# Performance work log

Hardware: AMD Instinct MI355X
Metric: run time of the kernel (lower is better)

The kernel has to match this reference:

```python
import jax, jax.numpy as jnp
import numpy as np

DN = ('NCHW', 'OIHW', 'NCHW')
LAP = jnp.array([[0., -1., 0.], [-1., 4., -1.], [0., -1., 0.]], dtype=jnp.float32).reshape(1, 1, 3, 3)
CH, NE = 24, 256


def conv(x, w, stride=1, pad=0):
    return jax.lax.conv_general_dilated(x, w, (stride, stride), ((pad, pad), (pad, pad)), dimension_numbers=DN)


def conv_t(x, w):
    # torch ConvTranspose2d(k=4, s=2, p=1); w is torch layout [in, out, 4, 4]
    wt = jnp.flip(w, (2, 3)).transpose(1, 0, 2, 3)
    return jax.lax.conv_general_dilated(x, wt, (1, 1), ((2, 2), (2, 2)), lhs_dilation=(2, 2), dimension_numbers=DN)


def spatial_attn(x, w_sa):
    y = jnp.concatenate([jnp.mean(x, 1, keepdims=True), jnp.max(x, 1, keepdims=True)], 1)
    return x * jax.nn.sigmoid(conv(y, w_sa, pad=3))


def res_branch(x, wr, wp, wsa):
    k = wr.shape[-1]
    h = conv(x, wr, pad=k // 2)
    h = conv(h, wp)
    return jax.nn.relu(spatial_attn(h, wsa))


def enc_block(x, wr, wp, wsa, wout):
    x = x + res_branch(x, wr, wp, wsa)
    return conv(x, wout, stride=2, pad=1)


def dec_block(x, wr, wp, wsa, wout):
    x = conv_t(x, wout)
    return x + res_branch(x, wr, wp, wsa)


def quantize(inp, embed):
    # inp: [B,H,W,D] tokens, embed: [D,N] codebook
    f = inp.reshape(-1, inp.shape[-1])
    dist = (f * f).sum(1, keepdims=True) - 2.0 * (f @ embed) + (embed * embed).sum(0, keepdims=True)
    ind = jnp.argmin(dist, axis=1)
    q = jnp.take(embed.T, ind, axis=0).reshape(inp.shape)
    diff = jnp.mean((jax.lax.stop_gradient(q) - inp) ** 2)
    q = inp + jax.lax.stop_gradient(q - inp)  # straight-through
    return q, diff


def _forward(x, w_img_in, w_img_out,
             w_res_et, w_pw_et, w_sa_et, w_out_et,
             w_res_em, w_pw_em, w_sa_em, w_out_em,
             w_res_ed, w_pw_ed, w_sa_ed, w_out_ed,
             w_res_dt, w_pw_dt, w_sa_dt, w_out_dt,
             w_res_dm, w_pw_dm, w_sa_dm, w_out_dm,
             w_res_dd, w_pw_dd, w_sa_dd, w_out_dd,
             w_squ1, w_squ2, embed2, embed3):
    xl = jax.lax.stop_gradient(conv(jnp.mean(x, 1, keepdims=True), LAP, pad=1))
    h = conv(xl, w_img_in)
    enc1 = enc_block(h, w_res_et, w_pw_et, w_sa_et, w_out_et)      # H/2
    enc2 = enc_block(enc1, w_res_em, w_pw_em, w_sa_em, w_out_em)   # H/4
    enc3 = enc_block(enc2, w_res_ed, w_pw_ed, w_sa_ed, w_out_ed)   # H/8
    qt2, d2 = quantize(enc2.transpose(0, 2, 3, 1), embed2)
    qt2 = qt2.transpose(0, 3, 1, 2)
    qt3, d3 = quantize(enc3.transpose(0, 2, 3, 1), embed3)
    qt3 = qt3.transpose(0, 3, 1, 2)
    dec3 = dec_block(qt3, w_res_dd, w_pw_dd, w_sa_dd, w_out_dd)    # H/4
    dec2 = conv(jnp.concatenate([dec3, qt2], 1), w_squ2)
    dec2 = dec_block(dec2, w_res_dm, w_pw_dm, w_sa_dm, w_out_dm)   # H/2
    dec1 = conv(jnp.concatenate([dec2, enc1], 1), w_squ1)
    dec1 = dec_block(dec1, w_res_dt, w_pw_dt, w_sa_dt, w_out_dt)   # H
    mask_lap = conv(dec1, w_img_out)
    clean_lap = xl - mask_lap
    return mask_lap, clean_lap, (d2 + d3).reshape(1)


def _param_shapes():
    shapes = {'w_img_in': (CH, 1, 1, 1), 'w_img_out': (1, CH, 1, 1),
              'w_squ1': (CH, 2 * CH, 1, 1), 'w_squ2': (CH, 2 * CH, 1, 1),
              'embed2': (CH, NE), 'embed3': (CH, NE)}
    for tag, k in [('et', 7), ('em', 5), ('ed', 3), ('dt', 7), ('dm', 5), ('dd', 3)]:
        shapes['w_res_' + tag] = (CH, CH, k, k)
        shapes['w_pw_' + tag] = (CH, CH, 1, 1)
        shapes['w_sa_' + tag] = (1, 2, 7, 7)
        shapes['w_out_' + tag] = (CH, CH, 4, 4)
    return shapes


def setup_inputs() -> dict:
    key = jax.random.key(0)
    shapes = _param_shapes()
    names = sorted(shapes)
    keys = jax.random.split(key, len(names) + 1)
    inputs = {'x': jax.random.normal(keys[0], (8, 3, 512, 512), dtype=jnp.float32)}
    for k_, name in zip(keys[1:], names):
        w = jax.random.normal(k_, shapes[name], dtype=jnp.float32)
        if not name.startswith('embed'):
            w = w * 0.05  # conv weight init scale
        inputs[name] = w
    return inputs


def reference(x, embed2, embed3, w_img_in, w_img_out,
              w_out_dd, w_out_dm, w_out_dt, w_out_ed, w_out_em, w_out_et,
              w_pw_dd, w_pw_dm, w_pw_dt, w_pw_ed, w_pw_em, w_pw_et,
              w_res_dd, w_res_dm, w_res_dt, w_res_ed, w_res_em, w_res_et,
              w_sa_dd, w_sa_dm, w_sa_dt, w_sa_ed, w_sa_em, w_sa_et,
              w_squ1, w_squ2):
    return _forward(x, w_img_in, w_img_out,
                    w_res_et, w_pw_et, w_sa_et, w_out_et,
                    w_res_em, w_pw_em, w_sa_em, w_out_em,
                    w_res_ed, w_pw_ed, w_sa_ed, w_out_ed,
                    w_res_dt, w_pw_dt, w_sa_dt, w_out_dt,
                    w_res_dm, w_pw_dm, w_sa_dm, w_out_dm,
                    w_res_dd, w_pw_dd, w_sa_dd, w_out_dd,
                    w_squ1, w_squ2, embed2, embed3)
```

## Files before the change

kernel.cpp:

```cpp
#include <hip/hip_runtime.h>
#include <math.h>

#define CH 24

typedef __attribute__((ext_vector_type(8))) short short8v;
typedef __attribute__((ext_vector_type(4))) float f32x4;
typedef unsigned short ushort_t;
typedef unsigned int uint_t;

__device__ inline ushort_t bf16r(float f){
  uint_t u = __float_as_uint(f);
  u += 0x7FFF + ((u>>16)&1);
  return (ushort_t)(u>>16);
}
__device__ inline float bf2f(uint_t u){ return __uint_as_float(u<<16); }

__global__ void k_r_res(const float* __restrict__ w, float* __restrict__ wT, int K){
  int i = blockIdx.x*256 + threadIdx.x;
  int n = 576*K*K; if (i >= n) return;
  int co = i % 24, ci = (i/24) % 24, kk = i/576;
  int ky = kk / K, kx = kk % K;
  wT[i] = w[((co*24+ci)*K+ky)*K+kx];
}
__global__ void k_r_pw(const float* __restrict__ w, float* __restrict__ wT, int CIN){
// ... 123 lines not shown
    for (int reg=0; reg<4; reg++){
      float v0 = acc[i][0][reg], v1 = acc[i][1][reg];
      float v0n = __shfl_xor(v0, 1, 64);
      float v1n = __shfl_xor(v1, 1, 64);
      int pxr = kg*4 + reg;
      uint_t packed; int uidx;
      if ((li & 1) == 0){
        packed = (uint_t)bf16r(v0) | ((uint_t)bf16r(v0n) << 16);
        uidx = li >> 1;
      } else {
        packed = (uint_t)bf16r(v1n) | ((uint_t)bf16r(v1) << 16);
        uidx = 8 + (li >> 1);
      }
      s[pxr*20 + uidx] = packed;
    }
    __asm__ volatile("s_waitcnt lgkmcnt(0)" ::: "memory");
    __builtin_amdgcn_sched_barrier(0);
    short8v a2 = *(const short8v*)((const ushort_t*)s + li*40 + kg*8);
    f32x4 d0 = __builtin_amdgcn_mfma_f32_16x16x32_bf16(a2, bpw0, zero, 0, 0, 0);
    f32x4 d1 = __builtin_amdgcn_mfma_f32_16x16x32_bf16(a2, bpw1, zero, 0, 0, 0);
    int gy = blockIdx.y*16 + wid + (i&1)*8;
    int gx = blockIdx.x*32 + (i>>1)*16 + kg*4;
    if (OUTBF){
      uint2 p0; p0.x = (uint_t)bf16r(d0[0]) | ((uint_t)bf16r(d0[1])<<16);
      p0.y = (uint_t)bf16r(d0[2]) | ((uint_t)bf16r(d0[3])<<16);
      *(uint2*)(outb_b + (size_t)li*HW + (size_t)gy*W + gx) = p0;
      if (li < 8){
        uint2 p1; p1.x = (uint_t)bf16r(d1[0]) | ((uint_t)bf16r(d1[1])<<16);
        p1.y = (uint_t)bf16r(d1[2]) | ((uint_t)bf16r(d1[3])<<16);
        *(uint2*)(outb_b + (size_t)(16+li)*HW + (size_t)gy*W + gx) = p1;
      }
    } else {
      *(f32x4*)(outb_f + (size_t)li*HW + (size_t)gy*W + gx) = d0;
      if (li < 8)
        *(f32x4*)(outb_f + (size_t)(16+li)*HW + (size_t)gy*W + gx) = d1;
    }
    f32x4 sm, mx;
    #pragma unroll
    for (int reg=0; reg<4; reg++){
      sm[reg] = d0[reg] + d1[reg];
      mx[reg] = fmaxf(d0[reg], (li<8) ? d1[reg] : -3.4e38f);
    }
    #pragma unroll
    for (int m=1; m<16; m<<=1){
      #pragma unroll
      for (int reg=0; reg<4; reg++){
        sm[reg] += __shfl_xor(sm[reg], m, 64);
        mx[reg] = fmaxf(mx[reg], __shfl_xor(mx[reg], m, 64));
      }
    }
    if (li == 0){
      f32x4 me; me[0]=sm[0]*(1.f/24.f); me[1]=sm[1]*(1.f/24.f); me[2]=sm[2]*(1.f/24.f); me[3]=sm[3]*(1.f/24.f);
      *(f32x4*)(mmb + (size_t)gy*W + gx) = me;
      *(f32x4*)(mmb + (size_t)HW + (size_t)gy*W + gx) = mx;
    }
  }
}

template<bool INBF, bool OUTBF>
__launch_bounds__(512)
__global__ void k_convT_mfma(const void* in, const ushort_t* __restrict__ wb,
                             void* out, int Ho, int Wo, int istrIn, int istrOut){
  const int Hi = Ho>>1, Wi = Wo>>1;
  constexpr int SW_T = 18, NPX = 180;
  __shared__ ushort_t lds[NPX*24];
  int tid = threadIdx.x;
  const float* inb_f = (const float*)in + (size_t)blockIdx.z*istrIn;
  const ushort_t* inb_b = (const ushort_t*)in + (size_t)blockIdx.z*istrIn;
  int X0 = blockIdx.x*32, Y0 = blockIdx.y*16;
  int ix0 = (X0>>1) - 1, iy0 = (Y0>>1) - 1;
  int HWi = Hi*Wi;
  for (int i = tid; i < NPX*3; i += 512){
    int q = i / NPX;
    int pp = i - q*NPX;
    int row = pp / SW_T, col = pp - row*SW_T;
    int gy = iy0 + row, gx = ix0 + col;
    uint4 w4; w4.x=0u; w4.y=0u; w4.z=0u; w4.w=0u;
    if (gy>=0 && gy<Hi && gx>=0 && gx<Wi){
      size_t base = (size_t)gy*Wi + gx;
      int c0 = q*8;
      if (INBF){
        uint_t u0=inb_b[(size_t)(c0+0)*HWi+base], u1=inb_b[(size_t)(c0+1)*HWi+base];
        uint_t u2=inb_b[(size_t)(c0+2)*HWi+base], u3=inb_b[(size_t)(c0+3)*HWi+base];
        uint_t u4=inb_b[(size_t)(c0+4)*HWi+base], u5=inb_b[(size_t)(c0+5)*HWi+base];
        uint_t u6=inb_b[(size_t)(c0+6)*HWi+base], u7=inb_b[(size_t)(c0+7)*HWi+base];
        w4.x = u0 | (u1<<16); w4.y = u2 | (u3<<16); w4.z = u4 | (u5<<16); w4.w = u6 | (u7<<16);
      } else {
        w4.x = (uint_t)bf16r(inb_f[(size_t)(c0+0)*HWi+base]) | ((uint_t)bf16r(inb_f[(size_t)(c0+1)*HWi+base])<<16);
        w4.y = (uint_t)bf16r(inb_f[(size_t)(c0+2)*HWi+base]) | ((uint_t)bf16r(inb_f[(size_t)(c0+3)*HWi+base])<<16);
        w4.z = (uint_t)bf16r(inb_f[(size_t)(c0+4)*HWi+base]) | ((uint_t)bf16r(inb_f[(size_t)(c0+5)*HWi+base])<<16);
        w4.w = (uint_t)bf16r(inb_f[(size_t)(c0+6)*HWi+base]) | ((uint_t)bf16r(inb_f[(size_t)(c0+7)*HWi+base])<<16);
      }
    }
    *(uint4*)(lds + (size_t)pp*24 + q*8) = w4;
  }
  __syncthreads();
  int l = tid & 63, wid = tid >> 6;
  int kg = l >> 4, li = l & 15;
  int kgc = (kg < 3) ? kg : 2;
  f32x4 zero = {0.f,0.f,0.f,0.f};
  f32x4 acc[4][2];
  #pragma unroll
  for (int i=0;i<4;i++){ acc[i][0]=zero; acc[i][1]=zero; }

  const ushort_t* aln = lds + li*24 + kgc*8;

  #pragma unroll
  for (int i=0;i<4;i++){
    int g = wid + 8*i;
    int r = g & 15, q = g >> 4;
    int ky0 = (r+1)&1;
    #pragma unroll
    for (int t2=0;t2<2;t2++){
      int ky = ky0 + 2*t2;
      int liy = ((r+1-ky)>>1) + 1;
      #pragma unroll
      for (int u=0;u<2;u++){
        int kx = (q ? 0 : 1) + 2*u;
        int lixb = ((q+1-kx)>>1) + 1;
        int tap = ky*4 + kx;
        const ushort_t* wp = wb + (size_t)tap*1024;
        short8v b0 = *(const short8v*)(wp + l*8);
        short8v b1 = *(const short8v*)(wp + 512 + l*8);
        short8v a = *(const short8v*)(aln + (liy*SW_T + lixb)*24);
        acc[i][0] = __builtin_amdgcn_mfma_f32_16x16x32_bf16(a, b0, acc[i][0], 0, 0, 0);
        acc[i][1] = __builtin_amdgcn_mfma_f32_16x16x32_bf16(a, b1, acc[i][1], 0, 0, 0);
      }
    }
  }
  float* outb_f = (float*)out + (size_t)blockIdx.z*istrOut;
  ushort_t* outb_b = (ushort_t*)out + (size_t)blockIdx.z*istrOut;
  int HWo = Ho*Wo;
  #pragma unroll
  for (int i=0;i<4;i++){
    int g = wid + 8*i;
    int r = g & 15, q = g >> 4;
    int oy = Y0 + r;
    #pragma unroll
    for (int reg=0; reg<4; reg++){
      int ox = X0 + 2*(kg*4 + reg) + q;
      if (OUTBF){
        outb_b[(size_t)li*HWo + (size_t)oy*Wo + ox] = bf16r(acc[i][0][reg]);
        if (li < 8)
          outb_b[(size_t)(16+li)*HWo + (size_t)oy*Wo + ox] = bf16r(acc[i][1][reg]);
      } else {
        outb_f[(size_t)li*HWo + (size_t)oy*Wo + ox] = acc[i][0][reg];
        if (li < 8)
          outb_f[(size_t)(16+li)*HWo + (size_t)oy*Wo + ox] = acc[i][1][reg];
      }
    }
  }
}

template<bool INBF>
__launch_bounds__(512)
__global__ void k_down_mfma(const void* in, const ushort_t* __restrict__ wb,
                            float* __restrict__ out, int Ho, int Wo, int istrIn, int istrOut){
  const int Hi = Ho*2, Wi = Wo*2;
  constexpr int NPX = 18*34;
  __shared__ ushort_t lds[NPX*24];
  int tid = threadIdx.x;
  const float* inb_f = (const float*)in + (size_t)blockIdx.z*istrIn;
  const ushort_t* inb_b = (const ushort_t*)in + (size_t)blockIdx.z*istrIn;
  int X0 = blockIdx.x*16, Y0 = blockIdx.y*8;
  int ix0 = 2*X0 - 1, iy0 = 2*Y0 - 1;
  int HWi = Hi*Wi;
  for (int i = tid; i < NPX*3; i += 512){
    int q = i / NPX;
    int pp = i - q*NPX;
    int row = pp / 34;
    int rem = pp - row*34;
    int par = (rem >= 17) ? 1 : 0;
    int sub = rem - par*17;
    int gx = ix0 + 2*sub + par;
    int gy = iy0 + row;
    uint4 w4; w4.x=0u; w4.y=0u; w4.z=0u; w4.w=0u;
    if (gy>=0 && gy<Hi && gx>=0 && gx<Wi){
      size_t base = (size_t)gy*Wi + gx;
      int c0 = q*8;
      if (INBF){
        uint_t u0=inb_b[(size_t)(c0+0)*HWi+base], u1=inb_b[(size_t)(c0+1)*HWi+base];
        uint_t u2=inb_b[(size_t)(c0+2)*HWi+base], u3=inb_b[(size_t)(c0+3)*HWi+base];
        uint_t u4=inb_b[(size_t)(c0+4)*HWi+base], u5=inb_b[(size_t)(c0+5)*HWi+base];
        uint_t u6=inb_b[(size_t)(c0+6)*HWi+base], u7=inb_b[(size_t)(c0+7)*HWi+base];
        w4.x = u0 | (u1<<16); w4.y = u2 | (u3<<16); w4.z = u4 | (u5<<16); w4.w = u6 | (u7<<16);
      } else {
        w4.x = (uint_t)bf16r(inb_f[(size_t)(c0+0)*HWi+base]) | ((uint_t)bf16r(inb_f[(size_t)(c0+1)*HWi+base])<<16);
        w4.y = (uint_t)bf16r(inb_f[(size_t)(c0+2)*HWi+base]) | ((uint_t)bf16r(inb_f[(size_t)(c0+3)*HWi+base])<<16);
        w4.z = (uint_t)bf16r(inb_f[(size_t)(c0+4)*HWi+base]) | ((uint_t)bf16r(inb_f[(size_t)(c0+5)*HWi+base])<<16);
        w4.w = (uint_t)bf16r(inb_f[(size_t)(c0+6)*HWi+base]) | ((uint_t)bf16r(inb_f[(size_t)(c0+7)*HWi+base])<<16);
      }
    }
    *(uint4*)(lds + (size_t)pp*24 + q*8) = w4;
  }
  __syncthreads();
  int l = tid & 63, wid = tid >> 6;
  int kg = l >> 4, li = l & 15;
  int kgc = (kg < 3) ? kg : 2;
  f32x4 zero = {0.f,0.f,0.f,0.f};
  f32x4 acc0 = zero, acc1 = zero;
  const ushort_t* aln = lds + li*24 + kgc*8 + (size_t)(2*wid)*34*24;
  #pragma unroll
  for (int ky=0; ky<4; ky++){
    #pragma unroll
    for (int kx=0; kx<4; kx++){
      int tap = ky*4 + kx;
      const ushort_t* wp = wb + (size_t)tap*1024;
      short8v b0 = *(const short8v*)(wp + l*8);
      short8v b1 = *(const short8v*)(wp + 512 + l*8);
      short8v a = *(const short8v*)(aln + (ky*34 + (kx&1)*17 + (kx>>1))*24);
      acc0 = __builtin_amdgcn_mfma_f32_16x16x32_bf16(a, b0, acc0, 0, 0, 0);
      acc1 = __builtin_amdgcn_mfma_f32_16x16x32_bf16(a, b1, acc1, 0, 0, 0);
    }
  }
  int HWo = Ho*Wo;
  float* outb = out + (size_t)blockIdx.z*istrOut;
  int oy = Y0 + wid, ox = X0 + kg*4;
  float* o0 = outb + (size_t)li*HWo + (size_t)oy*Wo + ox;
  *(f32x4*)o0 = acc0;
  if (li < 8){
    float* o1 = outb + (size_t)(16+li)*HWo + (size_t)oy*Wo + ox;
    *(f32x4*)o1 = acc1;
  }
}

template<int K, int TH>
__launch_bounds__(256)
__global__ void k_conv(const float* __restrict__ in, const float* __restrict__ wT,
                       float* __restrict__ out, int H, int W, int istrIn, int istrOut){
  constexpr int TW = 32;
  constexpr int PX = (TW*TH)/256;
  constexpr int XT = TW/PX;
  constexpr int SW = TW + K - 1;
  constexpr int SWP = SW | 1;
  constexpr int SH = TH + K - 1;
  constexpr int CC = 8;
  __shared__ float tile[CC*SH*SWP];
  int tx = threadIdx.x % XT, ty = threadIdx.x / XT;
  int x0 = blockIdx.x*TW - K/2, y0 = blockIdx.y*TH - K/2;
  const float* inb = in + (size_t)blockIdx.z*istrIn;
  float acc[CH][PX];
  #pragma unroll
  for (int co=0;co<CH;co++)
    #pragma unroll
    for (int px=0;px<PX;px++) acc[co][px] = 0.f;

  #pragma unroll 1
  for (int c0=0;c0<CH;c0+=CC){
    __syncthreads();
    for (int i=threadIdx.x; i<CC*SH*SW; i+=256){
      int col = i % SW; int rr = i / SW; int row = rr % SH; int c = rr / SH;
      int gy = y0+row, gx = x0+col;
      tile[(c*SH+row)*SWP+col] = (gy>=0 && gy<H && gx>=0 && gx<W)
          ? inb[(size_t)(c0+c)*H*W + (size_t)gy*W + gx] : 0.f;
    }
    __syncthreads();
    #pragma unroll 1
    for (int ci=0;ci<CC;ci++){
      #pragma unroll 1
      for (int ky=0;ky<K;ky++){
        const float* trow = &tile[(ci*SH + ty+ky)*SWP + tx*PX];
        #pragma unroll
        for (int kx=0;kx<K;kx++){
          float v[PX];
          #pragma unroll
          for (int px=0;px<PX;px++) v[px] = trow[kx+px];
          const float* wp = wT + ((ky*K+kx)*24 + c0+ci)*24;
          #pragma unroll
          for (int co=0;co<CH;co++){
            float wv = wp[co];
            #pragma unroll
            for (int px=0;px<PX;px++) acc[co][px] = fmaf(v[px], wv, acc[co][px]);
          }
        }
      }
    }
  }
  int oy = blockIdx.y*TH+ty, ox = blockIdx.x*TW+tx*PX;
  float* ob = out + (size_t)blockIdx.z*istrOut + (size_t)oy*W + ox;
  #pragma unroll
  for (int co=0;co<CH;co++){
    if (PX == 2){
      float2 o; o.x=acc[co][0]; o.y=acc[co][1];
      *(float2*)(ob + (size_t)co*H*W) = o;
    } else {
      ob[(size_t)co*H*W] = acc[co][0];
    }
  }
}

__global__ void k_pw(const float* in, const float* __restrict__ wT,
                     float* out, float* __restrict__ mm, int HW, int istr, int istrMM){
  int p = (blockIdx.x*256 + threadIdx.x)*4;
  if (p >= HW) return;
  const float* ib = in + (size_t)blockIdx.z*istr;
  float acc[CH][4];
  #pragma unroll
  for (int co=0;co<CH;co++){ acc[co][0]=0;acc[co][1]=0;acc[co][2]=0;acc[co][3]=0; }
  #pragma unroll 1
  for (int ci=0;ci<CH;ci++){
    float4 v = *(const float4*)(ib + (size_t)ci*HW + p);
    const float* wp = wT + ci*24;
    #pragma unroll
    for (int co=0;co<CH;co++){
      float wv = wp[co];
      acc[co][0] = fmaf(v.x, wv, acc[co][0]);
      acc[co][1] = fmaf(v.y, wv, acc[co][1]);
      acc[co][2] = fmaf(v.z, wv, acc[co][2]);
      acc[co][3] = fmaf(v.w, wv, acc[co][3]);
    }
  }
  float mean[4]={0,0,0,0}, mx[4]={-3.4e38f,-3.4e38f,-3.4e38f,-3.4e38f};
  #pragma unroll
  for (int co=0;co<CH;co++)
    #pragma unroll
    for (int j=0;j<4;j++){ mean[j]+=acc[co][j]; mx[j]=fmaxf(mx[j],acc[co][j]); }
  float* ob = out + (size_t)blockIdx.z*istr;
  #pragma unroll
  for (int co=0;co<CH;co++){
    float4 o; o.x=acc[co][0]; o.y=acc[co][1]; o.z=acc[co][2]; o.w=acc[co][3];
    *(float4*)(ob + (size_t)co*HW + p) = o;
  }
  float* mb = mm + (size_t)blockIdx.z*istrMM;
  float4 me; me.x=mean[0]*(1.f/24.f); me.y=mean[1]*(1.f/24.f); me.z=mean[2]*(1.f/24.f); me.w=mean[3]*(1.f/24.f);
  float4 mxo; mxo.x=mx[0]; mxo.y=mx[1]; mxo.z=mx[2]; mxo.w=mx[3];
  *(float4*)(mb + p) = me;
  *(float4*)(mb + HW + p) = mxo;
}

template<bool BF>
__global__ void k_attn_res(const void* R_, const float* __restrict__ M,
                           const void* X_, const float* __restrict__ wsa,
                           void* out_, int H, int W, int istr, int istrMM){
  int p = (blockIdx.x*256 + threadIdx.x)*4;
  int HW = H*W;
  if (p >= HW) return;
  int py = p / W, px0 = p % W;
  const float* Mb = M + (size_t)blockIdx.z*istrMM;
  float s[4]={0,0,0,0};
  #pragma unroll
  for (int cc=0;cc<2;cc++){
    const float* Mc = Mb + (size_t)cc*HW;
    #pragma unroll 1
    for (int ky=0;ky<7;ky++){
      int gy = py+ky-3;
      if (gy<0||gy>=H) continue;
      const float* mr = Mc + (size_t)gy*W;
      float mv[10];
      #pragma unroll
      for (int j=0;j<10;j++){
        int gx = px0-3+j;
        mv[j] = (gx>=0 && gx<W) ? mr[gx] : 0.f;
      }
      const float* wr = wsa + (cc*7+ky)*7;
      #pragma unroll
      for (int kx=0;kx<7;kx++){
        float wv = wr[kx];
        #pragma unroll
        for (int px=0;px<4;px++) s[px] = fmaf(mv[kx+px], wv, s[px]);
      }
    }
  }
  float g[4];
  #pragma unroll
  for (int px=0;px<4;px++) g[px] = 1.f/(1.f+expf(-s[px]));
  #pragma unroll
  for (int c=0;c<CH;c++){
    float r0,r1,r2,r3, x0v,x1v,x2v,x3v;
    if (BF){
      const ushort_t* Rb = (const ushort_t*)R_ + (size_t)blockIdx.z*istr + (size_t)c*HW + p;
      const ushort_t* Xb = (const ushort_t*)X_ + (size_t)blockIdx.z*istr + (size_t)c*HW + p;
      uint2 rv = *(const uint2*)Rb;
      uint2 xv = *(const uint2*)Xb;
      r0=bf2f(rv.x&0xffffu); r1=bf2f(rv.x>>16); r2=bf2f(rv.y&0xffffu); r3=bf2f(rv.y>>16);
      x0v=bf2f(xv.x&0xffffu); x1v=bf2f(xv.x>>16); x2v=bf2f(xv.y&0xffffu); x3v=bf2f(xv.y>>16);
    } else {
      const float* Rb = (const float*)R_ + (size_t)blockIdx.z*istr + (size_t)c*HW + p;
      const float* Xb = (const float*)X_ + (size_t)blockIdx.z*istr + (size_t)c*HW + p;
      float4 rv = *(const float4*)Rb;
      float4 xv = *(const float4*)Xb;
      r0=rv.x; r1=rv.y; r2=rv.z; r3=rv.w;
      x0v=xv.x; x1v=xv.y; x2v=xv.z; x3v=xv.w;
    }
    float o0 = x0v + fmaxf(r0*g[0], 0.f);
    float o1 = x1v + fmaxf(r1*g[1], 0.f);
    float o2 = x2v + fmaxf(r2*g[2], 0.f);
    float o3 = x3v + fmaxf(r3*g[3], 0.f);
    if (BF){
      ushort_t* Ob = (ushort_t*)out_ + (size_t)blockIdx.z*istr + (size_t)c*HW + p;
      uint2 ov;
      ov.x = (uint_t)bf16r(o0) | ((uint_t)bf16r(o1)<<16);
      ov.y = (uint_t)bf16r(o2) | ((uint_t)bf16r(o3)<<16);
      *(uint2*)Ob = ov;
    } else {
      float* Ob = (float*)out_ + (size_t)blockIdx.z*istr + (size_t)c*HW + p;
      float4 ov; ov.x=o0; ov.y=o1; ov.z=o2; ov.w=o3;
      *(float4*)Ob = ov;
    }
  }
}

template<bool BF>
__global__ void k_attn_res_x(const void* R_, const float* __restrict__ M,
                             const float* __restrict__ XL, const float* __restrict__ wsa,
                             const float* __restrict__ wexp,
                             void* out_, int H, int W, int istr, int istrMM){
  int p = (blockIdx.x*256 + threadIdx.x)*4;
  int HW = H*W;
  if (p >= HW) return;
  int py = p / W, px0 = p % W;
  const float* Mb = M + (size_t)blockIdx.z*istrMM;
  float s[4]={0,0,0,0};
  #pragma unroll
  for (int cc=0;cc<2;cc++){
    const float* Mc = Mb + (size_t)cc*HW;
    #pragma unroll 1
    for (int ky=0;ky<7;ky++){
      int gy = py+ky-3;
      if (gy<0||gy>=H) continue;
      const float* mr = Mc + (size_t)gy*W;
      float mv[10];
      #pragma unroll
      for (int j=0;j<10;j++){
        int gx = px0-3+j;
        mv[j] = (gx>=0 && gx<W) ? mr[gx] : 0.f;
      }
      const float* wr = wsa + (cc*7+ky)*7;
      #pragma unroll
      for (int kx=0;kx<7;kx++){
        float wv = wr[kx];
        #pragma unroll
        for (int px=0;px<4;px++) s[px] = fmaf(mv[kx+px], wv, s[px]);
      }
    }
  }
  float g[4];
  #pragma unroll
  for (int px=0;px<4;px++) g[px] = 1.f/(1.f+expf(-s[px]));
  float4 xl4 = *(const float4*)(XL + (size_t)blockIdx.z*HW + p);
  #pragma unroll
  for (int c=0;c<CH;c++){
    float wc = wexp[c];
    float r0,r1,r2,r3;
    if (BF){
      const ushort_t* Rb = (const ushort_t*)R_ + (size_t)blockIdx.z*istr + (size_t)c*HW + p;
      uint2 rv = *(const uint2*)Rb;
      r0=bf2f(rv.x&0xffffu); r1=bf2f(rv.x>>16); r2=bf2f(rv.y&0xffffu); r3=bf2f(rv.y>>16);
    } else {
      const float* Rb = (const float*)R_ + (size_t)blockIdx.z*istr + (size_t)c*HW + p;
      float4 rv = *(const float4*)Rb;
      r0=rv.x; r1=rv.y; r2=rv.z; r3=rv.w;
    }
    float o0 = xl4.x*wc + fmaxf(r0*g[0], 0.f);
    float o1 = xl4.y*wc + fmaxf(r1*g[1], 0.f);
    float o2 = xl4.z*wc + fmaxf(r2*g[2], 0.f);
    float o3 = xl4.w*wc + fmaxf(r3*g[3], 0.f);
    if (BF){
      ushort_t* Ob = (ushort_t*)out_ + (size_t)blockIdx.z*istr + (size_t)c*HW + p;
      uint2 ov;
      ov.x = (uint_t)bf16r(o0) | ((uint_t)bf16r(o1)<<16);
      ov.y = (uint_t)bf16r(o2) | ((uint_t)bf16r(o3)<<16);
      *(uint2*)Ob = ov;
    } else {
      float* Ob = (float*)out_ + (size_t)blockIdx.z*istr + (size_t)c*HW + p;
      float4 ov; ov.x=o0; ov.y=o1; ov.z=o2; ov.w=o3;
      *(float4*)Ob = ov;
    }
  }
}

__global__ void k_squeeze(const float* __restrict__ inA, const float* inB,
                          const float* __restrict__ wT, float* out, int HW, int istr){
  int p = (blockIdx.x*256 + threadIdx.x)*4;
  if (p >= HW) return;
  const float* Ab = inA + (size_t)blockIdx.z*istr;
  const float* Bb = inB + (size_t)blockIdx.z*istr;
  float acc[CH][4];
  #pragma unroll
  for (int co=0;co<CH;co++){ acc[co][0]=0;acc[co][1]=0;acc[co][2]=0;acc[co][3]=0; }
  #pragma unroll 1
  for (int ci=0;ci<48;ci++){
    const float* src = (ci<24) ? (Ab + (size_t)ci*HW) : (Bb + (size_t)(ci-24)*HW);
    float4 v = *(const float4*)(src + p);
    const float* wp = wT + ci*24;
    #pragma unroll
    for (int co=0;co<CH;co++){
      float wv = wp[co];
      acc[co][0] = fmaf(v.x, wv, acc[co][0]);
      acc[co][1] = fmaf(v.y, wv, acc[co][1]);
      acc[co][2] = fmaf(v.z, wv, acc[co][2]);
      acc[co][3] = fmaf(v.w, wv, acc[co][3]);
    }
  }
  float* ob = out + (size_t)blockIdx.z*istr;
  #pragma unroll
  for (int co=0;co<CH;co++){
    float4 o; o.x=acc[co][0]; o.y=acc[co][1]; o.z=acc[co][2]; o.w=acc[co][3];
    *(float4*)(ob + (size_t)co*HW + p) = o;
  }
}

__global__ void k_quant(const float* __restrict__ enc, const float* __restrict__ embed,
                        float* __restrict__ qt, float* __restrict__ diffAcc, int HW, int istr){
  __shared__ float em[256*28];
  __shared__ float red[4];
  {
    int j = threadIdx.x;
    float s = 0.f;
    #pragma unroll
    for (int c=0;c<CH;c++){
      float e = embed[c*256+j];
      em[j*28+c] = -2.0f*e;
      s = fmaf(e,e,s);
    }
    em[j*28+24] = s; em[j*28+25]=0.f; em[j*28+26]=0.f; em[j*28+27]=0.f;
  }
  __syncthreads();
  int p = blockIdx.x*256 + threadIdx.x;
  const float* eb = enc + (size_t)blockIdx.z*istr;
  float f[CH];
  #pragma unroll
  for (int c=0;c<CH;c++) f[c] = eb[(size_t)c*HW + p];
  float best = 3.4e38f; int bj = 0;
  #pragma unroll 1
  for (int j=0;j<256;j++){
    const float4* row = (const float4*)&em[j*28];
    float s = em[j*28+24];
    #pragma unroll
    for (int q4=0;q4<6;q4++){
      float4 r = row[q4];
      s = fmaf(f[q4*4+0], r.x, s);
      s = fmaf(f[q4*4+1], r.y, s);
      s = fmaf(f[q4*4+2], r.z, s);
      s = fmaf(f[q4*4+3], r.w, s);
    }
    if (s < best){ best = s; bj = j; }
  }
  float* qb = qt + (size_t)blockIdx.z*istr;
  float d = 0.f;
  #pragma unroll
  for (int c=0;c<CH;c++){
    float q = embed[c*256+bj];
    qb[(size_t)c*HW + p] = q;
    float e = q - f[c];
    d = fmaf(e,e,d);
  }
  #pragma unroll
  for (int off=32; off>0; off>>=1) d += __shfl_down(d, off, 64);
  int lane = threadIdx.x & 63, wv = threadIdx.x >> 6;
  if (lane==0) red[wv] = d;
  __syncthreads();
  if (threadIdx.x==0) atomicAdd(diffAcc, red[0]+red[1]+red[2]+red[3]);
}

__global__ void k_final(const ushort_t* __restrict__ dec1, const float* __restrict__ w,
                        const float* __restrict__ xl, float* __restrict__ outMask,
                        float* __restrict__ outClean, int HW, int dstr){
  int p = (blockIdx.x*256 + threadIdx.x)*4;
  if (p >= HW) return;
  const ushort_t* db = dec1 + (size_t)blockIdx.z*dstr;
  float m[4]={0,0,0,0};
  #pragma unroll
  for (int c=0;c<CH;c++){
    uint2 dv = *(const uint2*)(db + (size_t)c*HW + p);
    float wc = w[c];
    m[0]=fmaf(bf2f(dv.x&0xffffu),wc,m[0]);
    m[1]=fmaf(bf2f(dv.x>>16),wc,m[1]);
    m[2]=fmaf(bf2f(dv.y&0xffffu),wc,m[2]);
    m[3]=fmaf(bf2f(dv.y>>16),wc,m[3]);
  }
  float4 xv = *(const float4*)(xl + (size_t)blockIdx.z*HW + p);
  float4 mo; mo.x=m[0]; mo.y=m[1]; mo.z=m[2]; mo.w=m[3];
  float4 co; co.x=xv.x-m[0]; co.y=xv.y-m[1]; co.z=xv.z-m[2]; co.w=xv.w-m[3];
  *(float4*)(outMask + (size_t)blockIdx.z*HW + p) = mo;
  *(float4*)(outClean + (size_t)blockIdx.z*HW + p) = co;
}

__global__ void k_diff(const float* __restrict__ acc, float* __restrict__ out){
  out[0] = acc[0]*(1.f/3145728.f) + acc[1]*(1.f/786432.f);
}

extern "C" void kernel_launch(void* const* d_in, const int* in_sizes, int n_in,
                              void* d_out, int out_size, void* d_ws, size_t ws_size,
                              hipStream_t stream) {
  const float* x        = (const float*)d_in[0];
  const float* embed2   = (const float*)d_in[1];
  const float* embed3   = (const float*)d_in[2];
  const float* w_img_in = (const float*)d_in[3];
  const float* w_img_out= (const float*)d_in[4];
  const float* w_out_dd = (const float*)d_in[5];
  const float* w_out_dm = (const float*)d_in[6];
  const float* w_out_dt = (const float*)d_in[7];
  const float* w_out_ed = (const float*)d_in[8];
  const float* w_out_em = (const float*)d_in[9];
  const float* w_out_et = (const float*)d_in[10];
  const float* w_pw_dd  = (const float*)d_in[11];
  const float* w_pw_dm  = (const float*)d_in[12];
  const float* w_pw_dt  = (const float*)d_in[13];
  const float* w_pw_ed  = (const float*)d_in[14];
  const float* w_pw_em  = (const float*)d_in[15];
  const float* w_pw_et  = (const float*)d_in[16];
  const float* w_res_dd = (const float*)d_in[17];
  const float* w_res_dm = (const float*)d_in[18];
  const float* w_res_dt = (const float*)d_in[19];
  const float* w_res_ed = (const float*)d_in[20];
  const float* w_res_em = (const float*)d_in[21];
  const float* w_res_et = (const float*)d_in[22];
  const float* w_sa_dd  = (const float*)d_in[23];
  const float* w_sa_dm  = (const float*)d_in[24];
  const float* w_sa_dt  = (const float*)d_in[25];
  const float* w_sa_ed  = (const float*)d_in[26];
  const float* w_sa_em  = (const float*)d_in[27];
  const float* w_sa_et  = (const float*)d_in[28];
  const float* w_squ1   = (const float*)d_in[29];
  const float* w_squ2   = (const float*)d_in[30];
  (void)in_sizes; (void)n_in; (void)out_size;

  const int HW512 = 512*512, HW256 = 256*256, HW128 = 128*128, HW64 = 64*64;
  const int S512 = 24*HW512, S256 = 24*HW256, S128 = 24*HW128, S64 = 24*HW64;

  float* ws = (float*)d_ws;
  float* OUT = (float*)d_out;
  size_t F = ws_size / sizeof(float);

  float* WT      = ws;
  float* wt_ed3  = WT + 85248;
  float* wt_dd3  = WT + 90432;
  float* wt_pw_ed= WT + 152064;
  float* wt_pw_dd= WT + 152640;
  float* wt_squ1 = WT + 154368;
  float* wt_squ2 = WT + 155520;

  ushort_t* WB = (ushort_t*)(ws + 160000);
  ushort_t* wb_et7   = WB;
  ushort_t* wb_dt7   = WB + 50176;
  ushort_t* wb_em5   = WB + 100352;
  ushort_t* wb_dm5   = WB + 125952;
  ushort_t* wb_pw_et = WB + 151552;
  ushort_t* wb_pw_em = WB + 152576;
  ushort_t* wb_pw_dm = WB + 153600;
  ushort_t* wb_pw_dt = WB + 154624;
  ushort_t* wb4_dd   = WB + 155648;
  ushort_t* wb4_dm   = WB + 172032;
  ushort_t* wb4_dt   = WB + 188416;
  ushort_t* wb4d_et  = WB + 204800;
  ushort_t* wb4d_em  = WB + 221184;
  ushort_t* wb4d_ed  = WB + 237568;

  const size_t ABASE = 290000;

  auto needBatched = [&](size_t CB)->size_t{
    size_t u_f = ((CB*(size_t)S512 + 1)/2 > (size_t)8*S256) ? (CB*(size_t)S512+1)/2 : (size_t)8*S256;
    return ABASE + 2097152 + 12582912 + 3145728 + 786432 + CB*524288 + 2*u_f + 2;
  };
  int CB = 0;
  if (F >= needBatched(8)) CB = 8;
  else if (F >= needBatched(4)) CB = 4;
  else if (F >= needBatched(2)) CB = 2;
  const size_t NEED_B = ABASE + 15925250;
  if (CB == 0 && F < NEED_B) return;

  float *XL, *E1, *E2, *Q2, *E3, *Q3, *MM, *DIFF, *U1, *U2;
  if (CB > 0){
    size_t off = ABASE;
    size_t u_f = ((CB*(size_t)S512 + 1)/2 > (size_t)8*S256) ? (CB*(size_t)S512+1)/2 : (size_t)8*S256;
    XL = ws + off; off += 2097152;
    E1 = ws + off; off += 12582912;
    Q2 = ws + off; off += 3145728;
    Q3 = ws + off; off += 786432;
    MM = ws + off; off += CB*524288;
    U1 = ws + off; off += u_f;
    U2 = ws + off; off += u_f;
    DIFF = ws + off;
    E2 = OUT;
    E3 = OUT + 3145728;
  } else {
    size_t off = ABASE;
    XL = ws + off; off += 262144;
    U1 = ws + off; off += 6291456;
    U2 = ws + off; off += 6291456;
    E1 = ws + off; off += 1572864;
    E2 = ws + off; off += 393216;
    Q2 = ws + off; off += 393216;
    E3 = ws + off; off += 98304;
    Q3 = ws + off; off += 98304;
    MM = ws + off; off += 524288;
    DIFF = ws + off;
  }
  ushort_t* U1b = (ushort_t*)U1;
  ushort_t* U2b = (ushort_t*)U2;

  k_rmfma<<<dim3(196), 256, 0, stream>>>(w_res_et, wb_et7, 7);
  k_rmfma<<<dim3(196), 256, 0, stream>>>(w_res_dt, wb_dt7, 7);
  k_rmfma<<<dim3(100), 256, 0, stream>>>(w_res_em, wb_em5, 5);
  k_rmfma<<<dim3(100), 256, 0, stream>>>(w_res_dm, wb_dm5, 5);
  k_rmfma<<<dim3(4), 256, 0, stream>>>(w_pw_et, wb_pw_et, 1);
  k_rmfma<<<dim3(4), 256, 0, stream>>>(w_pw_em, wb_pw_em, 1);
  k_rmfma<<<dim3(4), 256, 0, stream>>>(w_pw_dm, wb_pw_dm, 1);
  k_rmfma<<<dim3(4), 256, 0, stream>>>(w_pw_dt, wb_pw_dt, 1);
  k_rmfma4<<<dim3(64), 256, 0, stream>>>(w_out_dd, wb4_dd);
  k_rmfma4<<<dim3(64), 256, 0, stream>>>(w_out_dm, wb4_dm);
  k_rmfma4<<<dim3(64), 256, 0, stream>>>(w_out_dt, wb4_dt);
  k_rmfma<<<dim3(64), 256, 0, stream>>>(w_out_et, wb4d_et, 4);
  k_rmfma<<<dim3(64), 256, 0, stream>>>(w_out_em, wb4d_em, 4);
  k_rmfma<<<dim3(64), 256, 0, stream>>>(w_out_ed, wb4d_ed, 4);
  k_r_res<<<dim3((576*9+255)/256), 256, 0, stream>>>(w_res_ed, wt_ed3, 3);
  k_r_res<<<dim3((576*9+255)/256), 256, 0, stream>>>(w_res_dd, wt_dd3, 3);
  k_r_pw<<<dim3(3), 256, 0, stream>>>(w_pw_ed, wt_pw_ed, 24);
  k_r_pw<<<dim3(3), 256, 0, stream>>>(w_pw_dd, wt_pw_dd, 24);
  k_r_pw<<<dim3(5), 256, 0, stream>>>(w_squ1, wt_squ1, 48);
  k_r_pw<<<dim3(5), 256, 0, stream>>>(w_squ2, wt_squ2, 48);

  hipMemsetAsync(DIFF, 0, 2*sizeof(float), stream);

  auto phase1 = [&](int c0, int nz, float* XLp, float* E1p){
    k_lap<<<dim3(HW512/256,1,nz), 256, 0, stream>>>(x + (size_t)c0*3*HW512, XLp, 512, 512);
    k_conv_mfma<7,true,false,true><<<dim3(16,32,nz), 512, 0, stream>>>(
        XLp, wb_et7, wb_pw_et, w_img_in, U2b, MM, 512, 512, HW512, S512, 2*HW512);
    k_attn_res_x<true><<<dim3(HW512/1024,1,nz), 256, 0, stream>>>(
        U2b, MM, XLp, w_sa_et, w_img_in, U1b, 512, 512, S512, 2*HW512);
    k_down_mfma<true><<<dim3(16,32,nz), 512, 0, stream>>>(U1b, wb4d_et, E1p, 256, 256, S512, S256);
  };

  auto deep = [&](int nb, float* E1p, float* SAp, float* SBp, float* E2p, float* Q2p,
                  float* E3p, float* Q3p, float* MMp, float* D1p){
    int mm256 = 2*HW256, mm128 = 2*HW128;
    k_conv_mfma<5,false,false,false><<<dim3(8,16,nb), 512, 0, stream>>>(
        E1p, wb_em5, wb_pw_em, nullptr, SAp, MMp, 256, 256, S256, S256, mm256);
    k_attn_res<false><<<dim3(HW256/1024,1,nb), 256, 0, stream>>>(SAp, MMp, E1p, w_sa_em, SBp, 256, 256, S256, mm256);
    k_down_mfma<false><<<dim3(8,16,nb), 512, 0, stream>>>(SBp, wb4d_em, E2p, 128, 128, S256, S128);
    k_conv<3,8><<<dim3(4,16,nb), 256, 0, stream>>>(E2p, wt_ed3, SAp, 128, 128, S128, S128);
    k_pw<<<dim3(HW128/1024,1,nb), 256, 0, stream>>>(SAp, wt_pw_ed, SAp, MMp, HW128, S128, mm128);
    k_attn_res<false><<<dim3(HW128/1024,1,nb), 256, 0, stream>>>(SAp, MMp, E2p, w_sa_ed, SBp, 128, 128, S128, mm128);
    k_down_mfma<false><<<dim3(4,8,nb), 512, 0, stream>>>(SBp, wb4d_ed, E3p, 64, 64, S128, S64);
    k_quant<<<dim3(HW128/256,1,nb), 256, 0, stream>>>(E2p, embed2, Q2p, DIFF+0, HW128, S128);
    k_quant<<<dim3(HW64/256,1,nb), 256, 0, stream>>>(E3p, embed3, Q3p, DIFF+1, HW64, S64);
    k_convT_mfma<false,false><<<dim3(4,8,nb), 512, 0, stream>>>(Q3p, wb4_dd, SAp, 128, 128, S64, S128);
    k_conv<3,8><<<dim3(4,16,nb), 256, 0, stream>>>(SAp, wt_dd3, SBp, 128, 128, S128, S128);
    k_pw<<<dim3(HW128/1024,1,nb), 256, 0, stream>>>(SBp, wt_pw_dd, SBp, MMp, HW128, S128, mm128);
    k_attn_res<false><<<dim3(HW128/1024,1,nb), 256, 0, stream>>>(SBp, MMp, SAp, w_sa_dd, SAp, 128, 128, S128, mm128);
    k_squeeze<<<dim3(HW128/1024,1,nb), 256, 0, stream>>>(SAp, Q2p, wt_squ2, SBp, HW128, S128);
    k_convT_mfma<false,false><<<dim3(8,16,nb), 512, 0, stream>>>(SBp, wb4_dm, SAp, 256, 256, S128, S256);
    k_conv_mfma<5,false,false,false><<<dim3(8,16,nb), 512, 0, stream>>>(
        SAp, wb_dm5, wb_pw_dm, nullptr, SBp, MMp, 256, 256, S256, S256, mm256);
    k_attn_res<false><<<dim3(HW256/1024,1,nb), 256, 0, stream>>>(SBp, MMp, SAp, w_sa_dm, SAp, 256, 256, S256, mm256);
    k_squeeze<<<dim3(HW256/1024,1,nb), 256, 0, stream>>>(SAp, E1p, wt_squ1, D1p, HW256, S256);
  };

  auto phase3 = [&](int c0, int nz, const float* D1p, const float* XLp){
    k_convT_mfma<false,true><<<dim3(16,32,nz), 512, 0, stream>>>(D1p, wb4_dt, U1b, 512, 512, S256, S512);
    k_conv_mfma<7,false,true,true><<<dim3(16,32,nz), 512, 0, stream>>>(
        U1b, wb_dt7, wb_pw_dt, nullptr, U2b, MM, 512, 512, S512, S512, 2*HW512);
    k_attn_res<true><<<dim3(HW512/1024,1,nz), 256, 0, stream>>>(U2b, MM, U1b, w_sa_dt, U1b, 512, 512, S512, 2*HW512);
    k_final<<<dim3(HW512/1024,1,nz), 256, 0, stream>>>(U1b, w_img_out, XLp,
                                                       OUT + (size_t)c0*HW512,
                                                       OUT + 2097152 + (size_t)c0*HW512,
                                                       HW512, S512);
  };

  if (CB > 0){
    for (int c0=0;c0<8;c0+=CB)
      phase1(c0, CB, XL + (size_t)c0*HW512, E1 + (size_t)c0*S256);
    deep(8, E1, U1, U2, E2, Q2, E3, Q3, MM, E1);
    for (int c0=0;c0<8;c0+=CB)
      phase3(c0, CB, E1 + (size_t)c0*S256, XL + (size_t)c0*HW512);
  } else {
    for (int b=0;b<8;b++){
      phase1(b, 1, XL, E1);
      deep(1, E1, U1, U2, E2, Q2, E3, Q3, MM, U2);
      phase3(b, 1, U2, XL);
    }
  }

  k_diff<<<1, 1, 0, stream>>>(DIFF, OUT + 4194304);
}
```

Measured before the change: 1.473 ms.

## Store 256-resolution activations in bf16 across the deep encoder/decoder path

Converts the H/2 (256x256) activation buffers (E1, the em/dm stage intermediates, the squeeze output) from fp32 to bf16 storage. Down-conv and squeeze kernels gain template flags for bf16 input and output, and the conv/attn/convT launches switch to their bf16 variants. This halves memory traffic and workspace at that resolution, which may allow a larger batch chunk CB. The cost is extra rounding error on the skip connection and decoder inputs.

New measurement: 1.440 ms. 1.02x faster.

```diff
diff --git a/kernel.cpp b/kernel.cpp
--- a/kernel.cpp
+++ b/kernel.cpp
@@ -299,10 +299,10 @@
   }
 }
 
-template<bool INBF>
+template<bool INBF, bool OUTBF>
 __launch_bounds__(512)
 __global__ void k_down_mfma(const void* in, const ushort_t* __restrict__ wb,
-                            float* __restrict__ out, int Ho, int Wo, int istrIn, int istrOut){
+                            void* out, int Ho, int Wo, int istrIn, int istrOut){
   const int Hi = Ho*2, Wi = Wo*2;
   constexpr int NPX = 18*34;
   __shared__ ushort_t lds[NPX*24];
@@ -361,13 +361,22 @@
     }
   }
   int HWo = Ho*Wo;
-  float* outb = out + (size_t)blockIdx.z*istrOut;
   int oy = Y0 + wid, ox = X0 + kg*4;
-  float* o0 = outb + (size_t)li*HWo + (size_t)oy*Wo + ox;
-  *(f32x4*)o0 = acc0;
-  if (li < 8){
-    float* o1 = outb + (size_t)(16+li)*HWo + (size_t)oy*Wo + ox;
-    *(f32x4*)o1 = acc1;
+  if (OUTBF){
+    ushort_t* outb = (ushort_t*)out + (size_t)blockIdx.z*istrOut;
+    uint2 p0; p0.x = (uint_t)bf16r(acc0[0]) | ((uint_t)bf16r(acc0[1])<<16);
+    p0.y = (uint_t)bf16r(acc0[2]) | ((uint_t)bf16r(acc0[3])<<16);
+    *(uint2*)(outb + (size_t)li*HWo + (size_t)oy*Wo + ox) = p0;
+    if (li < 8){
+      uint2 p1; p1.x = (uint_t)bf16r(acc1[0]) | ((uint_t)bf16r(acc1[1])<<16);
+      p1.y = (uint_t)bf16r(acc1[2]) | ((uint_t)bf16r(acc1[3])<<16);
+      *(uint2*)(outb + (size_t)(16+li)*HWo + (size_t)oy*Wo + ox) = p1;
+    }
+  } else {
+    float* outb = (float*)out + (size_t)blockIdx.z*istrOut;
+    *(f32x4*)(outb + (size_t)li*HWo + (size_t)oy*Wo + ox) = acc0;
+    if (li < 8)
+      *(f32x4*)(outb + (size_t)(16+li)*HWo + (size_t)oy*Wo + ox) = acc1;
   }
 }
 
@@ -616,34 +625,53 @@
   }
 }
 
-__global__ void k_squeeze(const float* __restrict__ inA, const float* inB,
-                          const float* __restrict__ wT, float* out, int HW, int istr){
+template<bool BF>
+__global__ void k_squeeze(const void* inA_, const void* inB_,
+                          const float* __restrict__ wT, void* out_, int HW, int istr){
   int p = (blockIdx.x*256 + threadIdx.x)*4;
   if (p >= HW) return;
-  const float* Ab = inA + (size_t)blockIdx.z*istr;
-  const float* Bb = inB + (size_t)blockIdx.z*istr;
   float acc[CH][4];
   #pragma unroll
   for (int co=0;co<CH;co++){ acc[co][0]=0;acc[co][1]=0;acc[co][2]=0;acc[co][3]=0; }
   #pragma unroll 1
   for (int ci=0;ci<48;ci++){
-    const float* src = (ci<24) ? (Ab + (size_t)ci*HW) : (Bb + (size_t)(ci-24)*HW);
-    float4 v = *(const float4*)(src + p);
+    float v0,v1,v2,v3;
+    if (BF){
+      const ushort_t* src = (ci<24)
+        ? ((const ushort_t*)inA_ + (size_t)blockIdx.z*istr + (size_t)ci*HW + p)
+        : ((const ushort_t*)inB_ + (size_t)blockIdx.z*istr + (size_t)(ci-24)*HW + p);
+      uint2 rv = *(const uint2*)src;
+      v0=bf2f(rv.x&0xffffu); v1=bf2f(rv.x>>16); v2=bf2f(rv.y&0xffffu); v3=bf2f(rv.y>>16);
+    } else {
+      const float* src = (ci<24)
+        ? ((const float*)inA_ + (size_t)blockIdx.z*istr + (size_t)ci*HW + p)
+        : ((const float*)inB_ + (size_t)blockIdx.z*istr + (size_t)(ci-24)*HW + p);
+      float4 rv = *(const float4*)src;
+      v0=rv.x; v1=rv.y; v2=rv.z; v3=rv.w;
+    }
     const float* wp = wT + ci*24;
     #pragma unroll
     for (int co=0;co<CH;co++){
       float wv = wp[co];
-      acc[co][0] = fmaf(v.x, wv, acc[co][0]);
-      acc[co][1] = fmaf(v.y, wv, acc[co][1]);
-      acc[co][2] = fmaf(v.z, wv, acc[co][2]);
-      acc[co][3] = fmaf(v.w, wv, acc[co][3]);
-    }
-  }
-  float* ob = out + (size_t)blockIdx.z*istr;
+      acc[co][0] = fmaf(v0, wv, acc[co][0]);
+      acc[co][1] = fmaf(v1, wv, acc[co][1]);
+      acc[co][2] = fmaf(v2, wv, acc[co][2]);
+      acc[co][3] = fmaf(v3, wv, acc[co][3]);
+    }
+  }
   #pragma unroll
   for (int co=0;co<CH;co++){
-    float4 o; o.x=acc[co][0]; o.y=acc[co][1]; o.z=acc[co][2]; o.w=acc[co][3];
-    *(float4*)(ob + (size_t)co*HW + p) = o;
+    if (BF){
+      ushort_t* ob = (ushort_t*)out_ + (size_t)blockIdx.z*istr + (size_t)co*HW + p;
+      uint2 ov;
+      ov.x = (uint_t)bf16r(acc[co][0]) | ((uint_t)bf16r(acc[co][1])<<16);
+      ov.y = (uint_t)bf16r(acc[co][2]) | ((uint_t)bf16r(acc[co][3])<<16);
+      *(uint2*)ob = ov;
+    } else {
+      float* ob = (float*)out_ + (size_t)blockIdx.z*istr + (size_t)co*HW + p;
+      float4 o; o.x=acc[co][0]; o.y=acc[co][1]; o.z=acc[co][2]; o.w=acc[co][3];
+      *(float4*)ob = o;
+    }
   }
 }
 
@@ -797,8 +825,10 @@
   const size_t ABASE = 290000;
 
   auto needBatched = [&](size_t CB)->size_t{
-    size_t u_f = ((CB*(size_t)S512 + 1)/2 > (size_t)8*S256) ? (CB*(size_t)S512+1)/2 : (size_t)8*S256;
-    return ABASE + 2097152 + 12582912 + 3145728 + 786432 + CB*524288 + 2*u_f + 2;
+    size_t u_f = (CB*(size_t)S512 + 1)/2;
+    if ((size_t)4*S256 > u_f) u_f = (size_t)4*S256;
+    if ((size_t)8*S128 > u_f) u_f = (size_t)8*S128;
+    return ABASE + 2097152 + (size_t)4*S256 + 3145728 + 786432 + CB*524288 + 2*u_f + 2;
   };
   int CB = 0;
   if (F >= needBatched(8)) CB = 8;
@@ -807,12 +837,15 @@
   const size_t NEED_B = ABASE + 15925250;
   if (CB == 0 && F < NEED_B) return;
 
-  float *XL, *E1, *E2, *Q2, *E3, *Q3, *MM, *DIFF, *U1, *U2;
+  float *XL, *E2, *Q2, *E3, *Q3, *MM, *DIFF, *U1, *U2;
+  ushort_t* E1b;
   if (CB > 0){
     size_t off = ABASE;
-    size_t u_f = ((CB*(size_t)S512 + 1)/2 > (size_t)8*S256) ? (CB*(size_t)S512+1)/2 : (size_t)8*S256;
+    size_t u_f = (CB*(size_t)S512 + 1)/2;
+    if ((size_t)4*S256 > u_f) u_f = (size_t)4*S256;
+    if ((size_t)8*S128 > u_f) u_f = (size_t)8*S128;
     XL = ws + off; off += 2097152;
-    E1 = ws + off; off += 12582912;
+    E1b = (ushort_t*)(ws + off); off += (size_t)4*S256;
     Q2 = ws + off; off += 3145728;
     Q3 = ws + off; off += 786432;
     MM = ws + off; off += CB*524288;
@@ -826,7 +859,7 @@
     XL = ws + off; off += 262144;
     U1 = ws + off; off += 6291456;
     U2 = ws + off; off += 6291456;
-    E1 = ws + off; off += 1572864;
+    E1b = (ushort_t*)(ws + off); off += 1572864;
     E2 = ws + off; off += 393216;
     Q2 = ws + off; off += 393216;
     E3 = ws + off; off += 98304;
@@ -860,42 +893,44 @@
 
   hipMemsetAsync(DIFF, 0, 2*sizeof(float), stream);
 
-  auto phase1 = [&](int c0, int nz, float* XLp, float* E1p){
+  auto phase1 = [&](int c0, int nz, float* XLp, ushort_t* E1p){
     k_lap<<<dim3(HW512/256,1,nz), 256, 0, stream>>>(x + (size_t)c0*3*HW512, XLp, 512, 512);
     k_conv_mfma<7,true,false,true><<<dim3(16,32,nz), 512, 0, stream>>>(
         XLp, wb_et7, wb_pw_et, w_img_in, U2b, MM, 512, 512, HW512, S512, 2*HW512);
     k_attn_res_x<true><<<dim3(HW512/1024,1,nz), 256, 0, stream>>>(
         U2b, MM, XLp, w_sa_et, w_img_in, U1b, 512, 512, S512, 2*HW512);
-    k_down_mfma<true><<<dim3(16,32,nz), 512, 0, stream>>>(U1b, wb4d_et, E1p, 256, 256, S512, S256);
+    k_down_mfma<true,true><<<dim3(16,32,nz), 512, 0, stream>>>(U1b, wb4d_et, E1p, 256, 256, S512, S256);
   };
 
-  auto deep = [&](int nb, float* E1p, float* SAp, float* SBp, float* E2p, float* Q2p,
-                  float* E3p, float* Q3p, float* MMp, float* D1p){
+  auto deep = [&](int nb, ushort_t* E1p, float* SAp, float* SBp, float* E2p, float* Q2p,
+                  float* E3p, float* Q3p, float* MMp, ushort_t* D1p){
+    ushort_t* SAb = (ushort_t*)SAp;
+    ushort_t* SBb = (ushort_t*)SBp;
     int mm256 = 2*HW256, mm128 = 2*HW128;
-    k_conv_mfma<5,false,false,false><<<dim3(8,16,nb), 512, 0, stream>>>(
-        E1p, wb_em5, wb_pw_em, nullptr, SAp, MMp, 256, 256, S256, S256, mm256);
-    k_attn_res<false><<<dim3(HW256/1024,1,nb), 256, 0, stream>>>(SAp, MMp, E1p, w_sa_em, SBp, 256, 256, S256, mm256);
-    k_down_mfma<false><<<dim3(8,16,nb), 512, 0, stream>>>(SBp, wb4d_em, E2p, 128, 128, S256, S128);
+    k_conv_mfma<5,false,true,true><<<dim3(8,16,nb), 512, 0, stream>>>(
+        E1p, wb_em5, wb_pw_em, nullptr, SAb, MMp, 256, 256, S256, S256, mm256);
+    k_attn_res<true><<<dim3(HW256/1024,1,nb), 256, 0, stream>>>(SAb, MMp, E1p, w_sa_em, SBb, 256, 256, S256, mm256);
+    k_down_mfma<true,false><<<dim3(8,16,nb), 512, 0, stream>>>(SBb, wb4d_em, E2p, 128, 128, S256, S128);
     k_conv<3,8><<<dim3(4,16,nb), 256, 0, stream>>>(E2p, wt_ed3, SAp, 128, 128, S128, S128);
     k_pw<<<dim3(HW128/1024,1,nb), 256, 0, stream>>>(SAp, wt_pw_ed, SAp, MMp, HW128, S128, mm128);
     k_attn_res<false><<<dim3(HW128/1024,1,nb), 256, 0, stream>>>(SAp, MMp, E2p, w_sa_ed, SBp, 128, 128, S128, mm128);
-    k_down_mfma<false><<<dim3(4,8,nb), 512, 0, stream>>>(SBp, wb4d_ed, E3p, 64, 64, S128, S64);
+    k_down_mfma<false,false><<<dim3(4,8,nb), 512, 0, stream>>>(SBp, wb4d_ed, E3p, 64, 64, S128, S64);
     k_quant<<<dim3(HW128/256,1,nb), 256, 0, stream>>>(E2p, embed2, Q2p, DIFF+0, HW128, S128);
     k_quant<<<dim3(HW64/256,1,nb), 256, 0, stream>>>(E3p, embed3, Q3p, DIFF+1, HW64, S64);
     k_convT_mfma<false,false><<<dim3(4,8,nb), 512, 0, stream>>>(Q3p, wb4_dd, SAp, 128, 128, S64, S128);
     k_conv<3,8><<<dim3(4,16,nb), 256, 0, stream>>>(SAp, wt_dd3, SBp, 128, 128, S128, S128);
     k_pw<<<dim3(HW128/1024,1,nb), 256, 0, stream>>>(SBp, wt_pw_dd, SBp, MMp, HW128, S128, mm128);
     k_attn_res<false><<<dim3(HW128/1024,1,nb), 256, 0, stream>>>(SBp, MMp, SAp, w_sa_dd, SAp, 128, 128, S128, mm128);
-    k_squeeze<<<dim3(HW128/1024,1,nb), 256, 0, stream>>>(SAp, Q2p, wt_squ2, SBp, HW128, S128);
-    k_convT_mfma<false,false><<<dim3(8,16,nb), 512, 0, stream>>>(SBp, wb4_dm, SAp, 256, 256, S128, S256);
-    k_conv_mfma<5,false,false,false><<<dim3(8,16,nb), 512, 0, stream>>>(
-        SAp, wb_dm5, wb_pw_dm, nullptr, SBp, MMp, 256, 256, S256, S256, mm256);
-    k_attn_res<false><<<dim3(HW256/1024,1,nb), 256, 0, stream>>>(SBp, MMp, SAp, w_sa_dm, SAp, 256, 256, S256, mm256);
-    k_squeeze<<<dim3(HW256/1024,1,nb), 256, 0, stream>>>(SAp, E1p, wt_squ1, D1p, HW256, S256);
+    k_squeeze<false><<<dim3(HW128/1024,1,nb), 256, 0, stream>>>(SAp, Q2p, wt_squ2, SBp, HW128, S128);
+    k_convT_mfma<false,true><<<dim3(8,16,nb), 512, 0, stream>>>(SBp, wb4_dm, SAb, 256, 256, S128, S256);
+    k_conv_mfma<5,false,true,true><<<dim3(8,16,nb), 512, 0, stream>>>(
+        SAb, wb_dm5, wb_pw_dm, nullptr, SBb, MMp, 256, 256, S256, S256, mm256);
+    k_attn_res<true><<<dim3(HW256/1024,1,nb), 256, 0, stream>>>(SBb, MMp, SAb, w_sa_dm, SAb, 256, 256, S256, mm256);
+    k_squeeze<true><<<dim3(HW256/1024,1,nb), 256, 0, stream>>>(SAb, E1p, wt_squ1, D1p, HW256, S256);
   };
 
-  auto phase3 = [&](int c0, int nz, const float* D1p, const float* XLp){
-    k_convT_mfma<false,true><<<dim3(16,32,nz), 512, 0, stream>>>(D1p, wb4_dt, U1b, 512, 512, S256, S512);
+  auto phase3 = [&](int c0, int nz, const ushort_t* D1p, const float* XLp){
+    k_convT_mfma<true,true><<<dim3(16,32,nz), 512, 0, stream>>>(D1p, wb4_dt, U1b, 512, 512, S256, S512);
     k_conv_mfma<7,false,true,true><<<dim3(16,32,nz), 512, 0, stream>>>(
         U1b, wb_dt7, wb_pw_dt, nullptr, U2b, MM, 512, 512, S512, S512, 2*HW512);
     k_attn_res<true><<<dim3(HW512/1024,1,nz), 256, 0, stream>>>(U2b, MM, U1b, w_sa_dt, U1b, 512, 512, S512, 2*HW512);
@@ -907,15 +942,15 @@
 
   if (CB > 0){
     for (int c0=0;c0<8;c0+=CB)
-      phase1(c0, CB, XL + (size_t)c0*HW512, E1 + (size_t)c0*S256);
-    deep(8, E1, U1, U2, E2, Q2, E3, Q3, MM, E1);
+      phase1(c0, CB, XL + (size_t)c0*HW512, E1b + (size_t)c0*S256);
+    deep(8, E1b, U1, U2, E2, Q2, E3, Q3, MM, E1b);
     for (int c0=0;c0<8;c0+=CB)
-      phase3(c0, CB, E1 + (size_t)c0*S256, XL + (size_t)c0*HW512);
+      phase3(c0, CB, E1b + (size_t)c0*S256, XL + (size_t)c0*HW512);
   } else {
     for (int b=0;b<8;b++){
-      phase1(b, 1, XL, E1);
-      deep(1, E1, U1, U2, E2, Q2, E3, Q3, MM, U2);
-      phase3(b, 1, U2, XL);
+      phase1(b, 1, XL, E1b);
+      deep(1, E1b, U1, U2, E2, Q2, E3, Q3, MM, (ushort_t*)U2);
+      phase3(b, 1, (ushort_t*)U2, XL);
     }
   }
 
```
